# Kernel optimization log

Hardware: AMD Instinct MI355X
Metric: run time of the kernel (lower is better)

## Reference

```python
import jax, jax.numpy as jnp
import numpy as np

B, T, H = 4, 4096, 4096


def setup_inputs() -> dict:
    key = jax.random.key(0)
    k1, k2, k3, k4 = jax.random.split(key, 4)
    # activations scaled so several burst iterations would be needed per element
    x = jax.random.normal(k1, (B, T, H), dtype=jnp.float32) * 2.0
    mem = jax.random.normal(k2, (B, T, H), dtype=jnp.float32)
    # threshold strictly positive, per hidden channel
    threshold = jax.random.uniform(k3, (H,), dtype=jnp.float32, minval=0.5, maxval=1.5)
    # spike_count is always a non-negative integer multiple of threshold
    # (it starts at 0 and is only ever incremented/decremented by threshold)
    counts = jax.random.randint(k4, (B, T, H), 0, 4).astype(jnp.float32)
    spike_count = counts * threshold  # broadcast [H] over [B,T,H]
    return {"x": x, "mem": mem, "spike_count": spike_count, "threshold": threshold}


def reference(x, mem, spike_count, threshold):
    """One burst-mode CIF step. Closed form of the two while-loops:

    loop1: while mem > th:  mem -= th; spike += th; sc += th
    loop2: while (mem < -th) and (sc > 0): mem += th; spike -= th; sc -= th
    Returns spike (the module's forward output).
    """
    th = threshold  # [H], broadcasts over [B,T,H]
    m = mem + x
    # number of positive burst iterations: smallest k with m - k*th <= th
    k_pos = jnp.maximum(jnp.ceil((m - th) / th), 0.0)
    m1 = m - k_pos * th  # membrane after positive loop (<= th)
    # available negative-spike budget in units of th (sc is an exact multiple)
    sc_units = jnp.round((spike_count + k_pos * th) / th)
    # iterations needed so that m1 + j*th >= -th
    j_mem = jnp.maximum(jnp.ceil((-m1 - th) / th), 0.0)
    k_neg = jnp.minimum(j_mem, jnp.maximum(sc_units, 0.0))
    spike = (k_pos - k_neg) * th
    return spike
```

## Files before the change

### kernel.cpp

```cpp
#include <hip/hip_runtime.h>


__device__ __forceinline__ float cif_one(float xv, float mv, float sv, float t) {
    float m = __fadd_rn(mv, xv);
    float kpos = fmaxf(ceilf(__fdiv_rn(__fsub_rn(m, t), t)), 0.0f);
    float kpt = __fmul_rn(kpos, t);
    float m1  = __fsub_rn(m, kpt);
    float sc_units = rintf(__fdiv_rn(__fadd_rn(sv, kpt), t));
    float jmem = fmaxf(ceilf(__fdiv_rn(__fsub_rn(-m1, t), t)), 0.0f);
    float kneg = fminf(jmem, fmaxf(sc_units, 0.0f));
    return __fmul_rn(__fsub_rn(kpos, kneg), t);
}

__global__ __launch_bounds__(256) void CIFNeuron_36558761624015_kernel(
        const float4* __restrict__ x,
        const float4* __restrict__ mem,
        const float4* __restrict__ sc,
        const float*  __restrict__ th,
        float4* __restrict__ out,
        long long n4, int hmask ) {
    long long stride = (long long)gridDim.x * blockDim.x;
    for (long long i = (long long)blockIdx.x * blockDim.x + threadIdx.x;
         i < n4; i += stride) {
        float4 xv = x[i];
        float4 mv = mem[i];
        float4 sv = sc[i];
        int h = (int)((i * 4) & (long long)hmask);
        float4 tv = *reinterpret_cast<const float4*>(th + h);
        float4 o;
        o.x = cif_one(xv.x, mv.x, sv.x, tv.x);
        o.y = cif_one(xv.y, mv.y, sv.y, tv.y);
        o.z = cif_one(xv.z, mv.z, sv.z, tv.z);
        o.w = cif_one(xv.w, mv.w, sv.w, tv.w);
        out[i] = o;
    }
}

extern "C" void kernel_launch(void* const* d_in, const int* in_sizes, int n_in,
                              void* d_out, int out_size, void* d_ws, size_t ws_size,
                              hipStream_t stream) {
    const float* x   = (const float*)d_in[0];
    const float* mem = (const float*)d_in[1];
    const float* sc  = (const float*)d_in[2];
    const float* th  = (const float*)d_in[3];
    float* out = (float*)d_out;

    const int H = in_sizes[3];
    long long n  = (long long)out_size;
    long long n4 = n / 4;

    int threads = 256;
    long long want = (n4 + threads - 1) / threads;
    int blocks = (int)((want < 2048) ? want : 2048);

    CIFNeuron_36558761624015_kernel<<<blocks, threads, 0, stream>>>(
        (const float4*)x, (const float4*)mem, (const float4*)sc, th,
        (float4*)out, n4, H - 1);
}
```

Before: 219.1 us.

## Unroll loads per thread, use nontemporal stores, and replace one divide with reciprocal

Replaces the grid-stride loop with a fixed grid where each thread handles four float4 groups, issuing all loads before compute to raise memory-level parallelism. Output is written with nontemporal stores to avoid polluting cache. One of the three divisions is replaced by a hardware reciprocal multiply, which is approximate but is followed by rounding, so results should be robust since sc is an exact multiple of threshold. The grid now scales with problem size instead of being capped at 2048 blocks.

Result: faster. 187.0 us (-14.7%).

```diff
diff --git a/kernel.cpp b/kernel.cpp
--- a/kernel.cpp
+++ b/kernel.cpp
@@ -1,38 +1,64 @@
 #include <hip/hip_runtime.h>
 
+
+typedef float v4f __attribute__((ext_vector_type(4)));
+
+constexpr int TPB = 256;
+constexpr int UF  = 4;
 
 __device__ __forceinline__ float cif_one(float xv, float mv, float sv, float t) {
     float m = __fadd_rn(mv, xv);
     float kpos = fmaxf(ceilf(__fdiv_rn(__fsub_rn(m, t), t)), 0.0f);
     float kpt = __fmul_rn(kpos, t);
     float m1  = __fsub_rn(m, kpt);
-    float sc_units = rintf(__fdiv_rn(__fadd_rn(sv, kpt), t));
+    float rt = __builtin_amdgcn_rcpf(t);
+    float sc_units = rintf(__fmul_rn(__fadd_rn(sv, kpt), rt));
     float jmem = fmaxf(ceilf(__fdiv_rn(__fsub_rn(-m1, t), t)), 0.0f);
     float kneg = fminf(jmem, fmaxf(sc_units, 0.0f));
     return __fmul_rn(__fsub_rn(kpos, kneg), t);
 }
 
-__global__ __launch_bounds__(256) void CIFNeuron_36558761624015_kernel(
+__global__ __launch_bounds__(TPB) void CIFNeuron_36558761624015_kernel(
         const float4* __restrict__ x,
         const float4* __restrict__ mem,
         const float4* __restrict__ sc,
         const float*  __restrict__ th,
         float4* __restrict__ out,
         long long n4, int hmask ) {
-    long long stride = (long long)gridDim.x * blockDim.x;
-    for (long long i = (long long)blockIdx.x * blockDim.x + threadIdx.x;
-         i < n4; i += stride) {
-        float4 xv = x[i];
-        float4 mv = mem[i];
-        float4 sv = sc[i];
-        int h = (int)((i * 4) & (long long)hmask);
-        float4 tv = *reinterpret_cast<const float4*>(th + h);
-        float4 o;
-        o.x = cif_one(xv.x, mv.x, sv.x, tv.x);
-        o.y = cif_one(xv.y, mv.y, sv.y, tv.y);
-        o.z = cif_one(xv.z, mv.z, sv.z, tv.z);
-        o.w = cif_one(xv.w, mv.w, sv.w, tv.w);
-        out[i] = o;
+    long long base = (long long)blockIdx.x * (TPB * UF) + threadIdx.x;
+
+    float4 xv[UF], mv[UF], sv[UF], tv[UF];
+    bool ok[UF];
+
+    #pragma unroll
+    for (int k = 0; k < UF; ++k) {
+        long long i = base + (long long)k * TPB;
+        ok[k] = (i < n4);
+        if (ok[k]) {
+            xv[k] = x[i];
+            mv[k] = mem[i];
+            sv[k] = sc[i];
+        }
+    }
+    #pragma unroll
+    for (int k = 0; k < UF; ++k) {
+        if (ok[k]) {
+            long long i = base + (long long)k * TPB;
+            int h = (int)((i * 4) & (long long)hmask);
+            tv[k] = *reinterpret_cast<const float4*>(th + h);
+        }
+    }
+    #pragma unroll
+    for (int k = 0; k < UF; ++k) {
+        if (ok[k]) {
+            long long i = base + (long long)k * TPB;
+            v4f o;
+            o.x = cif_one(xv[k].x, mv[k].x, sv[k].x, tv[k].x);
+            o.y = cif_one(xv[k].y, mv[k].y, sv[k].y, tv[k].y);
+            o.z = cif_one(xv[k].z, mv[k].z, sv[k].z, tv[k].z);
+            o.w = cif_one(xv[k].w, mv[k].w, sv[k].w, tv[k].w);
+            __builtin_nontemporal_store(o, reinterpret_cast<v4f*>(out + i));
+        }
     }
 }
 
@@ -49,11 +75,10 @@
     long long n  = (long long)out_size;
     long long n4 = n / 4;
 
-    int threads = 256;
-    long long want = (n4 + threads - 1) / threads;
-    int blocks = (int)((want < 2048) ? want : 2048);
+    long long per_block = (long long)TPB * UF;
+    int blocks = (int)((n4 + per_block - 1) / per_block);
 
-    CIFNeuron_36558761624015_kernel<<<blocks, threads, 0, stream>>>(
+    CIFNeuron_36558761624015_kernel<<<blocks, TPB, 0, stream>>>(
         (const float4*)x, (const float4*)mem, (const float4*)sc, th,
         (float4*)out, n4, H - 1);
 }
```

## Unroll loads per thread, use nontemporal stores, and replace grid-stride loop

Applied to the files above, without the earlier changes.

Replaces the capped grid-stride loop with one block per 1024 float4 chunks, where each thread issues four batched loads of each input before computing, to raise memory-level parallelism. Output writes use nontemporal stores to avoid polluting cache with streamed data. One division is replaced with a hardware reciprocal multiply, which can change rounding in the sc_units computation, though rint absorbs it. A separate tail kernel handles leftover elements.

After: 189.8 us. 13.4% less time.

```diff
diff --git a/kernel.cpp b/kernel.cpp
--- a/kernel.cpp
+++ b/kernel.cpp
@@ -1,38 +1,71 @@
 #include <hip/hip_runtime.h>
 
+
+typedef float v4f __attribute__((ext_vector_type(4)));
+
+constexpr int TPB = 256;
+constexpr int UF  = 4;
 
 __device__ __forceinline__ float cif_one(float xv, float mv, float sv, float t) {
     float m = __fadd_rn(mv, xv);
     float kpos = fmaxf(ceilf(__fdiv_rn(__fsub_rn(m, t), t)), 0.0f);
     float kpt = __fmul_rn(kpos, t);
     float m1  = __fsub_rn(m, kpt);
-    float sc_units = rintf(__fdiv_rn(__fadd_rn(sv, kpt), t));
+    float rt = __builtin_amdgcn_rcpf(t);
+    float sc_units = rintf(__fmul_rn(__fadd_rn(sv, kpt), rt));
     float jmem = fmaxf(ceilf(__fdiv_rn(__fsub_rn(-m1, t), t)), 0.0f);
     float kneg = fminf(jmem, fmaxf(sc_units, 0.0f));
     return __fmul_rn(__fsub_rn(kpos, kneg), t);
 }
 
-__global__ __launch_bounds__(256) void CIFNeuron_36558761624015_kernel(
+__device__ __forceinline__ v4f cif_vec(float4 xv, float4 mv, float4 sv, float4 tv) {
+    v4f o;
+    o.x = cif_one(xv.x, mv.x, sv.x, tv.x);
+    o.y = cif_one(xv.y, mv.y, sv.y, tv.y);
+    o.z = cif_one(xv.z, mv.z, sv.z, tv.z);
+    o.w = cif_one(xv.w, mv.w, sv.w, tv.w);
+    return o;
+}
+
+__global__ __launch_bounds__(TPB) void CIFNeuron_36558761624015_main(
         const float4* __restrict__ x,
         const float4* __restrict__ mem,
         const float4* __restrict__ sc,
         const float*  __restrict__ th,
         float4* __restrict__ out,
-        long long n4, int hmask ) {
-    long long stride = (long long)gridDim.x * blockDim.x;
-    for (long long i = (long long)blockIdx.x * blockDim.x + threadIdx.x;
-         i < n4; i += stride) {
-        float4 xv = x[i];
-        float4 mv = mem[i];
-        float4 sv = sc[i];
+        int hmask ) {
+    const long long base = (long long)blockIdx.x * (TPB * UF) + threadIdx.x;
+
+    float4 xv[UF], mv[UF], sv[UF];
+    #pragma unroll
+    for (int k = 0; k < UF; ++k) xv[k] = x[base + (long long)k * TPB];
+    #pragma unroll
+    for (int k = 0; k < UF; ++k) mv[k] = mem[base + (long long)k * TPB];
+    #pragma unroll
+    for (int k = 0; k < UF; ++k) sv[k] = sc[base + (long long)k * TPB];
+
+    #pragma unroll
+    for (int k = 0; k < UF; ++k) {
+        int h = (int)(((base + (long long)k * TPB) * 4) & (long long)hmask);
+        float4 tv = *reinterpret_cast<const float4*>(th + h);
+        v4f o = cif_vec(xv[k], mv[k], sv[k], tv);
+        __builtin_nontemporal_store(o, reinterpret_cast<v4f*>(out) + base + (long long)k * TPB);
+    }
+}
+
+__global__ __launch_bounds__(TPB) void CIFNeuron_36558761624015_tail(
+        const float4* __restrict__ x,
+        const float4* __restrict__ mem,
+        const float4* __restrict__ sc,
+        const float*  __restrict__ th,
+        float4* __restrict__ out,
+        long long start, long long n4, int hmask) {
+    long long i = start + (long long)blockIdx.x * TPB + threadIdx.x;
+    if (i < n4) {
         int h = (int)((i * 4) & (long long)hmask);
         float4 tv = *reinterpret_cast<const float4*>(th + h);
-        float4 o;
-        o.x = cif_one(xv.x, mv.x, sv.x, tv.x);
-        o.y = cif_one(xv.y, mv.y, sv.y, tv.y);
-        o.z = cif_one(xv.z, mv.z, sv.z, tv.z);
-        o.w = cif_one(xv.w, mv.w, sv.w, tv.w);
-        out[i] = o;
+        v4f o = cif_vec(x[i], mem[i], sc[i], tv);
+        __builtin_nontemporal_store(o, reinterpret_cast<v4f*>(out) + i);
     }
 }
 
@@ -49,11 +82,19 @@
     long long n  = (long long)out_size;
     long long n4 = n / 4;
 
-    int threads = 256;
-    long long want = (n4 + threads - 1) / threads;
-    int blocks = (int)((want < 2048) ? want : 2048);
+    const long long per_block = (long long)TPB * UF;
+    long long full_blocks = n4 / per_block;
+    long long rem_chunks  = n4 - full_blocks * per_block;
 
-    CIFNeuron_36558761624015_kernel<<<blocks, threads, 0, stream>>>(
-        (const float4*)x, (const float4*)mem, (const float4*)sc, th,
-        (float4*)out, n4, H - 1);
+    if (full_blocks > 0) {
+        CIFNeuron_36558761624015_main<<<(int)full_blocks, TPB, 0, stream>>>(
+            (const float4*)x, (const float4*)mem, (const float4*)sc, th,
+            (float4*)out, H - 1);
+    }
+    if (rem_chunks > 0) {
+        int tail_blocks = (int)((rem_chunks + TPB - 1) / TPB);
+        CIFNeuron_36558761624015_tail<<<tail_blocks, TPB, 0, stream>>>(
+            (const float4*)x, (const float4*)mem, (const float4*)sc, th,
+            (float4*)out, full_blocks * per_block, n4, H - 1);
+    }
 }
```
